# Performance work log

Hardware: AMD Instinct MI355X
Metric: run time of the kernel (lower is better)

Reference implementation:

```python
import jax, jax.numpy as jnp
import numpy as np

D = 1024
H = 16
HD = D // H
DS = 64
B, L = 2, 2048


def setup_inputs() -> dict:
    key = jax.random.key(0)
    ks = jax.random.split(key, 12)
    s = 0.02
    return {
        "x": jax.random.normal(ks[0], (B, L, D), jnp.float32),
        "subject_embed": jax.random.normal(ks[1], (B, DS), jnp.float32),
        "key_padding_mask": jnp.zeros((B, L), jnp.bool_),
        "Wq": jax.random.normal(ks[2], (D, D), jnp.float32) * s,
        "Wk": jax.random.normal(ks[3], (D, D), jnp.float32) * s,
        "Wv": jax.random.normal(ks[4], (D, D), jnp.float32) * s,
        "Wo": jax.random.normal(ks[5], (D, D), jnp.float32) * s,
        "bo": jnp.zeros((D,), jnp.float32),
        "Wsq": jax.random.normal(ks[6], (DS, D), jnp.float32) * s,
        "bsq": jnp.zeros((D,), jnp.float32),
        "Wsk": jax.random.normal(ks[7], (DS, D), jnp.float32) * s,
        "bsk": jnp.zeros((D,), jnp.float32),
    }


def reference(x, subject_embed, key_padding_mask, Wq, Wk, Wv, Wo, bo, Wsq, bsq, Wsk, bsk):
    scale = 1.0 / jnp.sqrt(jnp.asarray(HD, x.dtype))
    q = x @ Wq + (subject_embed @ Wsq + bsq)[:, None, :]   # [B,L,D]
    k = x @ Wk + (subject_embed @ Wsk + bsk)[:, None, :]
    v = x @ Wv
    # split heads: [B,H,L,hd]
    q = q.reshape(B, L, H, HD).transpose(0, 2, 1, 3)
    k = k.reshape(B, L, H, HD).transpose(0, 2, 1, 3)
    v = v.reshape(B, L, H, HD).transpose(0, 2, 1, 3)
    attn = jnp.einsum('bhqd,bhkd->bhqk', q, k) * scale      # [B,H,L,L]
    attn = jnp.where(key_padding_mask[:, None, None, :], -jnp.inf, attn)
    attn = jax.nn.softmax(attn, axis=-1)
    out = jnp.einsum('bhqk,bhkd->bhqd', attn, v)
    out = out.transpose(0, 2, 1, 3).reshape(B, L, D)
    return out @ Wo + bo
```

## Files before the change

kernel.cpp:

```cpp
#include <hip/hip_runtime.h>
#include <hip/hip_bf16.h>
#include <math.h>

#define DEV __device__ __forceinline__

typedef short bf16x8 __attribute__((ext_vector_type(8)));
typedef short bf16x4 __attribute__((ext_vector_type(4)));
typedef float f32x4 __attribute__((ext_vector_type(4)));

static constexpr int D  = 1024;
static constexpr int H  = 16;
static constexpr int HD = 64;
static constexpr int DS = 64;
static constexpr int B  = 2;
static constexpr int L  = 2048;
static constexpr int M  = B * L;

static constexpr float QSCALE = 0.18033688011112042f;

DEV unsigned short f2bf(float f) {
  union { float f; unsigned u; } x; x.f = f;
  unsigned r = (x.u + 0x7FFFu + ((x.u >> 16) & 1u)) >> 16;
  return (unsigned short)r;
}

DEV unsigned pack2bf(float a, float b) {
  return (unsigned)f2bf(a) | ((unsigned)f2bf(b) << 16);
}

DEV unsigned pack2bf_trunc(float a, float b) {
  union { float f; unsigned u; } ua{a}, ub{b};
  return __builtin_amdgcn_perm(ub.u, ua.u, 0x07060302u);
}

DEV void gload_lds16(const void* g, void* l) {
  __builtin_amdgcn_global_load_lds(
      (const __attribute__((address_space(1))) unsigned int*)g,
      (__attribute__((address_space(3))) unsigned int*)l, 16, 0, 0);
}

__global__ __launch_bounds__(256) void prep_kernel(
    const float* __restrict__ Wq, const float* __restrict__ Wk,
    const float* __restrict__ Wv, const float* __restrict__ Wo,
    const float* __restrict__ x, const float* __restrict__ subj,
    const float* __restrict__ Wsq, const float* __restrict__ bsq,
    const float* __restrict__ Wsk, const float* __restrict__ bsk,
    unsigned short* __restrict__ WT4, unsigned short* __restrict__ xb,
    float* __restrict__ sq, float* __restrict__ sk) {
  __shared__ float tile[64][65];
  const int blk = blockIdx.x, t = threadIdx.x;
  if (blk < 1024) {
    const int z = blk >> 8, idx = blk & 255;
    const float* W = z == 0 ? Wq : z == 1 ? Wk : z == 2 ? Wv : Wo;
    unsigned short* dst = WT4 + (size_t)z * D * D;
    const int n0 = (idx & 15) * 64, k0 = (idx >> 4) * 64;
    const int c = t & 63, r4 = t >> 6;
#pragma unroll
    for (int rr = 0; rr < 16; ++rr) {
      int row = r4 + rr * 4;
      tile[row][c] = W[(size_t)(k0 + row) * D + n0 + c];
    }
    __syncthreads();
#pragma unroll
    for (int rr = 0; rr < 16; ++rr) {
      int nrow = r4 + rr * 4;
      dst[(size_t)(n0 + nrow) * D + k0 + c] = f2bf(tile[c][nrow]);
    }
  } else if (blk < 3072) {
    size_t g = (size_t)(blk - 1024) * 256 + t;
    const float4* xf = (const float4*)x;
    float4 a = xf[2 * g], b = xf[2 * g + 1];
    union { unsigned short s[8]; uint4 v; } o;
    o.s[0] = f2bf(a.x); o.s[1] = f2bf(a.y); o.s[2] = f2bf(a.z); o.s[3] = f2bf(a.w);
    o.s[4] = f2bf(b.x); o.s[5] = f2bf(b.y); o.s[6] = f2bf(b.z); o.s[7] = f2bf(b.w);
    ((uint4*)xb)[g] = o.v;
  } else {
    int g = (blk - 3072) * 256 + t;
    int ty = g >> 11, b = (g >> 10) & 1, n = g & 1023;
    const float* W = ty ? Wsk : Wsq;
    const float* bias = ty ? bsk : bsq;
    float s = bias[n];
#pragma unroll 8
    for (int d = 0; d < DS; ++d) s += subj[b * DS + d] * W[d * D + n];
    (ty ? sk : sq)[b * D + n] = s;
  }
}

__global__ __launch_bounds__(256) void proj_kernel(
    const unsigned short* __restrict__ xb, const unsigned short* __restrict__ WT3,
    const float* __restrict__ sq, const float* __restrict__ sk,
    unsigned short* __restrict__ qk, unsigned short* __restrict__ vT) {
  __shared__ __align__(16) unsigned short smem[32768];
  const int lin = blockIdx.x + 8 * (blockIdx.y + 32 * blockIdx.z);
  const int nlin = (lin & 7) * 96 + (lin >> 3);
  const int z = nlin >> 8;
  const int rem = nlin & 255;
  const unsigned short* Wt = WT3 + (size_t)z * D * D;
  const int m0 = (rem >> 3) * 128, n0 = (rem & 7) * 128;
  const int t = threadIdx.x, l = t & 63, w = t >> 6;
  const int wm = w >> 1, wn = w & 1;
  const int lm = l & 15, lq = l >> 4;
  const int srow8 = t >> 3;
  const int fsw = ((t & 7) ^ ((t >> 3) & 7)) * 8;
  const int swm = lm & 7;

  auto stage = [&](int kt, int bsel) {
    const int kb = kt * 64;
    unsigned short* As = smem + bsel * 16384;
    unsigned short* Bs = As + 8192;
#pragma unroll
    for (int c = 0; c < 4; ++c) {
      int row = 32 * c + srow8;
      gload_lds16(&xb[(size_t)(m0 + row) * D + kb + fsw], &As[(32 * c + 8 * w) * 64]);
      gload_lds16(&Wt[(size_t)(n0 + row) * D + kb + fsw], &Bs[(32 * c + 8 * w) * 64]);
    }
  };

  f32x4 acc[4][4] = {};
  stage(0, 0);
  __syncthreads();
  for (int kt = 0; kt < D / 64; ++kt) {
    const int cur = kt & 1;
    if (kt + 1 < D / 64) stage(kt + 1, cur ^ 1);
    const unsigned short* As = smem + cur * 16384;
    const unsigned short* Bs = As + 8192;
#pragma unroll
    for (int kk = 0; kk < 2; ++kk) {
      bf16x8 af[4], bf[4];
#pragma unroll
      for (int i = 0; i < 4; ++i)
        af[i] = *(const bf16x8*)&As[(64 * wm + 16 * i + lm) * 64 + ((kk * 4 + lq) ^ swm) * 8];
#pragma unroll
      for (int j = 0; j < 4; ++j)
        bf[j] = *(const bf16x8*)&Bs[(64 * wn + 16 * j + lm) * 64 + ((kk * 4 + lq) ^ swm) * 8];
#pragma unroll
      for (int i = 0; i < 4; ++i)
#pragma unroll
        for (int j = 0; j < 4; ++j)
          acc[i][j] = __builtin_amdgcn_mfma_f32_16x16x32_bf16(af[i], bf[j], acc[i][j], 0, 0, 0);
    }
    __syncthreads();
  }
  if (z == 2) {
#pragma unroll
    for (int i = 0; i < 4; ++i)
#pragma unroll
      for (int j = 0; j < 4; ++j) {
        int cr = 64 * wn + 16 * j + lm;
        int rr = 64 * wm + 16 * i + 4 * lq;
        uint2 u;
        u.x = pack2bf(acc[i][j][0], acc[i][j][1]);
        u.y = pack2bf(acc[i][j][2], acc[i][j][3]);
        *(uint2*)&smem[cr * 136 + rr] = u;
      }
    __syncthreads();
    const int cr = t >> 1, half = t & 1;
    const int bb = m0 >> 11, l0 = m0 & (L - 1);
    const int gcol = n0 + cr, h = gcol >> 6, hd = gcol & 63;
    size_t dbase = ((size_t)(bb * H + h) * HD + hd) * L + l0 + half * 64;
#pragma unroll
    for (int c = 0; c < 8; ++c) {
      uint4 u = *(const uint4*)&smem[cr * 136 + half * 64 + c * 8];
      *(uint4*)&vT[dbase + c * 8] = u;
    }
  } else {
    unsigned short* dst = qk + (size_t)z * M * D;
    const float* bias = z == 0 ? sq : sk;
    const float post = z == 0 ? QSCALE : 1.0f;
#pragma unroll
    for (int i = 0; i < 4; ++i)
#pragma unroll
      for (int j = 0; j < 4; ++j)
#pragma unroll
        for (int r = 0; r < 4; ++r) {
          int rr = 64 * wm + 16 * i + 4 * lq + r;
          int cc = 64 * wn + 16 * j + lm;
          float v = (acc[i][j][r] + bias[((m0 + rr) >> 11) * D + n0 + cc]) * post;
          smem[rr * 136 + cc] = f2bf(v);
        }
    __syncthreads();
    const int row = t >> 1, half = t & 1;
    const int bb = m0 >> 11, ll = (m0 & (L - 1)) + row;
    const int h0 = (n0 >> 6) + half;
    size_t dbase = ((size_t)(bb * H + h0) * L + ll) * HD;
#pragma unroll
    for (int c = 0; c < 8; ++c) {
      uint4 u = *(const uint4*)&smem[row * 136 + half * 64 + c * 8];
      *(uint4*)&dst[dbase + c * 8] = u;
    }
  }
}

__global__ __launch_bounds__(512, 4) void attn_kernel(
    const unsigned short* __restrict__ q_hm, const unsigned short* __restrict__ k_hm,
    const unsigned short* __restrict__ vT, const unsigned char* __restrict__ mask,
    unsigned short* __restrict__ ctx) {
  __shared__ __align__(16) unsigned short smem[40960];
  unsigned short* Qs  = smem;
  unsigned short* Ksb = smem + 8192;
  unsigned short* Vtb = smem + 24576;
  const int bx = blockIdx.x;
  const int rest = bx >> 3;
  const int bhid = (bx & 7) + 8 * (rest >> 4);
  const int q0 = (rest & 15) * 128;
  const int h = bhid & 15, b = bhid >> 4;
  const size_t bh = (size_t)(b * H + h);
  const unsigned short* qp = q_hm + bh * L * HD;
  const unsigned short* kp = k_hm + bh * L * HD;
  const unsigned short* vp = vT + bh * HD * L;
  const int t = threadIdx.x, l = t & 63, w = t >> 6;
  const int wq = w & 3, wj = w >> 2;
  const int lm = l & 15, lq = l >> 4;
  const int fsw = ((t & 7) ^ ((t >> 3) & 7)) * 8;
  const int swm = lm & 7;
  const int srow = t >> 3;
  const int vs = t & 15, vr = t >> 4;
  const int vcsrc = ((vs & 8) | ((vs & 7) ^ (vr & 7))) * 8;
  const int krow0 = 8 * (lm >> 2) + 4 * ((lm >> 2) & 1) + (lm & 3);
  const int ks0 = krow0 & 7;
  const int krow1 = krow0 ^ 4;
  const int ks1 = ks0 ^ 4;
  const bf16x8 vones = {(short)0x3F80, (short)0x3F80, (short)0x3F80, (short)0x3F80,
                        (short)0x3F80, (short)0x3F80, (short)0x3F80, (short)0x3F80};

#pragma unroll
  for (int c = 0; c < 2; ++c) {
    gload_lds16(&qp[(size_t)(q0 + 64 * c + srow) * HD + fsw], &Qs[(64 * c + 8 * w) * 64]);
    gload_lds16(&kp[(size_t)(64 * c + srow) * HD + fsw], &Ksb[(64 * c + 8 * w) * 64]);
    gload_lds16(&vp[(size_t)(32 * c + vr) * L + vcsrc], &Vtb[(32 * c + 4 * w) * 128]);
  }
  __syncthreads();
  bf16x8 qf[2][2];
#pragma unroll
  for (int i = 0; i < 2; ++i)
#pragma unroll
    for (int kk = 0; kk < 2; ++kk)
      qf[i][kk] = *(const bf16x8*)&Qs[(wq * 32 + 16 * i + lm) * 64 + ((kk * 4 + lq) ^ swm) * 8];

  f32x4 ot[2][4] = {};
  f32x4 ot1[2] = {};

  for (int kt = 0; kt < L / 128; ++kt) {
    const int cur = kt & 1;
    const unsigned short* Kc = Ksb + cur * 8192;
    const unsigned short* Vc = Vtb + cur * 8192;
    unsigned char mby = mask[b * L + kt * 128 + 64 * wj + l];
    if (kt + 1 < L / 128) {
      const int nk0 = (kt + 1) * 128;
      unsigned short* Kd = Ksb + (cur ^ 1) * 8192;
      unsigned short* Vd = Vtb + (cur ^ 1) * 8192;
#pragma unroll
      for (int c = 0; c < 2; ++c) {
        gload_lds16(&kp[(size_t)(nk0 + 64 * c + srow) * HD + fsw], &Kd[(64 * c + 8 * w) * 64]);
        gload_lds16(&vp[(size_t)(32 * c + vr) * L + nk0 + vcsrc], &Vd[(32 * c + 4 * w) * 128]);
      }
    }
    unsigned long long mb = __ballot(mby != 0);

#pragma unroll
    for (int g = 0; g < 2; ++g) {
      const int gg = 2 * wj + g;
      const unsigned short* Kg = Kc + 32 * gg * 64;
      bf16x8 ka0 = *(const bf16x8*)&Kg[krow0 * 64 + ((0 + lq) ^ ks0) * 8];
      bf16x8 ka1 = *(const bf16x8*)&Kg[krow0 * 64 + ((4 + lq) ^ ks0) * 8];
      bf16x8 kb0 = *(const bf16x8*)&Kg[krow1 * 64 + ((0 + lq) ^ ks1) * 8];
      bf16x8 kb1 = *(const bf16x8*)&Kg[krow1 * 64 + ((4 + lq) ^ ks1) * 8];
      f32x4 stA[2], stB[2];
      __builtin_amdgcn_s_setprio(1);
#pragma unroll
      for (int i = 0; i < 2; ++i) {
        f32x4 a = {};
        a = __builtin_amdgcn_mfma_f32_16x16x32_bf16(ka0, qf[i][0], a, 0, 0, 0);
        a = __builtin_amdgcn_mfma_f32_16x16x32_bf16(ka1, qf[i][1], a, 0, 0, 0);
        stA[i] = a;
        f32x4 bq = {};
        bq = __builtin_amdgcn_mfma_f32_16x16x32_bf16(kb0, qf[i][0], bq, 0, 0, 0);
        bq = __builtin_amdgcn_mfma_f32_16x16x32_bf16(kb1, qf[i][1], bq, 0, 0, 0);
        stB[i] = bq;
      }
      __builtin_amdgcn_s_setprio(0);
      if (mb) {
        const int shA = 32 * g + 8 * lq + 4 * (lq & 1);
        unsigned bitsA = (unsigned)(mb >> shA);
        unsigned bitsB = (unsigned)(mb >> (shA ^ 4));
#pragma unroll
        for (int i = 0; i < 2; ++i)
#pragma unroll
          for (int r = 0; r < 4; ++r) {
            if ((bitsA >> r) & 1u) stA[i][r] = -1e30f;
            if ((bitsB >> r) & 1u) stB[i][r] = -1e30f;
          }
      }
      union { uint4 q; bf16x8 v; } pa[2];
      const bool sw = (lq & 1) != 0;
#pragma unroll
      for (int i = 0; i < 2; ++i) {
        float eA[4], eB[4];
#pragma unroll
        for (int r = 0; r < 4; ++r) {
          eA[r] = __builtin_amdgcn_exp2f(stA[i][r]);
          eB[r] = __builtin_amdgcn_exp2f(stB[i][r]);
        }
        unsigned a01 = pack2bf_trunc(eA[0], eA[1]);
        unsigned a23 = pack2bf_trunc(eA[2], eA[3]);
        unsigned b01 = pack2bf_trunc(eB[0], eB[1]);
        unsigned b23 = pack2bf_trunc(eB[2], eB[3]);
        pa[i].q.x = sw ? b01 : a01;
        pa[i].q.y = sw ? b23 : a23;
        pa[i].q.z = sw ? a01 : b01;
        pa[i].q.w = sw ? a23 : b23;
      }
      const int kc = 4 * gg + lq;
      const int slot = (kc & 8) | ((kc & 7) ^ swm);
      __builtin_amdgcn_s_setprio(1);
#pragma unroll
      for (int jf = 0; jf < 4; ++jf) {
        bf16x8 vb = *(const bf16x8*)&Vc[(16 * jf + lm) * 128 + slot * 8];
#pragma unroll
        for (int i = 0; i < 2; ++i)
          ot[i][jf] = __builtin_amdgcn_mfma_f32_16x16x32_bf16(pa[i].v, vb, ot[i][jf], 0, 0, 0);
      }
#pragma unroll
      for (int i = 0; i < 2; ++i)
        ot1[i] = __builtin_amdgcn_mfma_f32_16x16x32_bf16(pa[i].v, vones, ot1[i], 0, 0, 0);
      __builtin_amdgcn_s_setprio(0);
    }
    __syncthreads();
  }

  float* Obuf = (float*)smem;
  unsigned short* Es = smem + 20480;
  float* Sred = (float*)(smem + 35840);

  if (lm == 0) {
#pragma unroll
    for (int i = 0; i < 2; ++i)
#pragma unroll
      for (int r = 0; r < 4; ++r)
        Sred[w * 32 + 16 * i + 4 * lq + r] = ot1[i][r];
  }
  if (wj) {
#pragma unroll
    for (int i = 0; i < 2; ++i)
#pragma unroll
      for (int jf = 0; jf < 4; ++jf)
        *(f32x4*)&Obuf[(16 * jf + lm) * 132 + wq * 32 + 16 * i + 4 * lq] = ot[i][jf];
  }
  __syncthreads();
  if (!wj) {
    float rlq[2][4];
#pragma unroll
    for (int i = 0; i < 2; ++i)
#pragma unroll
      for (int r = 0; r < 4; ++r)
        rlq[i][r] = 1.0f / (ot1[i][r] + Sred[(w + 4) * 32 + 16 * i + 4 * lq + r]);
#pragma unroll
    for (int i = 0; i < 2; ++i)
#pragma unroll
      for (int jf = 0; jf < 4; ++jf) {
        f32x4 po = *(const f32x4*)&Obuf[(16 * jf + lm) * 132 + wq * 32 + 16 * i + 4 * lq];
        ot[i][jf] += po;
      }
#pragma unroll
    for (int i = 0; i < 2; ++i)
#pragma unroll
      for (int jf = 0; jf < 4; ++jf)
#pragma unroll
        for (int r = 0; r < 4; ++r)
          Es[(wq * 32 + 16 * i + 4 * lq + r) * 72 + 16 * jf + lm] =
              f2bf(ot[i][jf][r] * rlq[i][r]);
    int row = l >> 1, half = l & 1;
    size_t obase = ((size_t)(b * L + q0 + wq * 32 + row)) * D + h * HD + half * 32;
#pragma unroll
    for (int c = 0; c < 4; ++c) {
      uint4 u = *(const uint4*)&Es[(wq * 32 + row) * 72 + half * 32 + c * 8];
      *(uint4*)&ctx[obase + c * 8] = u;
    }
  }
}

__global__ __launch_bounds__(256) void outgemm_kernel(
    const unsigned short* __restrict__ ctx, const unsigned short* __restrict__ WoT,
    const float* __restrict__ bo, float* __restrict__ out) {
  __shared__ __align__(16) unsigned short smem[24576];
  const int lin = blockIdx.x + 8 * blockIdx.y;
  const int nlin = (lin & 7) * 64 + (lin >> 3);
  const int m0 = (nlin >> 3) * 64, n0 = (nlin & 7) * 128;
  const int t = threadIdx.x, l = t & 63, w = t >> 6;
  const int wm = w >> 1, wn = w & 1;
  const int lm = l & 15, lq = l >> 4;
  const int srow8 = t >> 3;
  const int fsw = ((t & 7) ^ ((t >> 3) & 7)) * 8;
  const int swm = lm & 7;

  auto stage = [&](int kt, int bsel) {
    const int kb = kt * 64;
    unsigned short* As = smem + bsel * 12288;
    unsigned short* Bs = As + 4096;
#pragma unroll
    for (int c = 0; c < 2; ++c)
      gload_lds16(&ctx[(size_t)(m0 + 32 * c + srow8) * D + kb + fsw],
                  &As[(32 * c + 8 * w) * 64]);
#pragma unroll
    for (int c = 0; c < 4; ++c)
      gload_lds16(&WoT[(size_t)(n0 + 32 * c + srow8) * D + kb + fsw],
                  &Bs[(32 * c + 8 * w) * 64]);
  };

  f32x4 acc[2][4] = {};
  stage(0, 0);
  __syncthreads();
  for (int kt = 0; kt < D / 64; ++kt) {
    const int cur = kt & 1;
    if (kt + 1 < D / 64) stage(kt + 1, cur ^ 1);
    const unsigned short* As = smem + cur * 12288;
    const unsigned short* Bs = As + 4096;
#pragma unroll
    for (int kk = 0; kk < 2; ++kk) {
      bf16x8 af[2], bf[4];
#pragma unroll
      for (int i = 0; i < 2; ++i)
        af[i] = *(const bf16x8*)&As[(32 * wm + 16 * i + lm) * 64 + ((kk * 4 + lq) ^ swm) * 8];
#pragma unroll
      for (int j = 0; j < 4; ++j)
        bf[j] = *(const bf16x8*)&Bs[(64 * wn + 16 * j + lm) * 64 + ((kk * 4 + lq) ^ swm) * 8];
#pragma unroll
      for (int i = 0; i < 2; ++i)
#pragma unroll
        for (int j = 0; j < 4; ++j)
          acc[i][j] = __builtin_amdgcn_mfma_f32_16x16x32_bf16(af[i], bf[j], acc[i][j], 0, 0, 0);
    }
    __syncthreads();
  }
#pragma unroll
  for (int i = 0; i < 2; ++i)
#pragma unroll
    for (int j = 0; j < 4; ++j)
#pragma unroll
      for (int r = 0; r < 4; ++r) {
        int grow = m0 + 32 * wm + 16 * i + lq * 4 + r;
        int gcol = n0 + 64 * wn + 16 * j + lm;
        out[(size_t)grow * D + gcol] = acc[i][j][r] + bo[gcol];
      }
}

extern "C" void kernel_launch(void* const* d_in, const int* in_sizes, int n_in,
                              void* d_out, int out_size, void* d_ws, size_t ws_size,
                              hipStream_t stream) {
  const float* x    = (const float*)d_in[0];
  const float* subj = (const float*)d_in[1];
  const unsigned char* mask = (const unsigned char*)d_in[2];
  const float* Wq = (const float*)d_in[3];
  const float* Wk = (const float*)d_in[4];
  const float* Wv = (const float*)d_in[5];
  const float* Wo = (const float*)d_in[6];
  const float* bo = (const float*)d_in[7];
  const float* Wsq = (const float*)d_in[8];
  const float* bsq = (const float*)d_in[9];
  const float* Wsk = (const float*)d_in[10];
  const float* bsk = (const float*)d_in[11];
  float* out = (float*)d_out;
  char* ws = (char*)d_ws;

  unsigned short* xb  = (unsigned short*)(ws);
  unsigned short* WT4 = (unsigned short*)(ws + (8ull  << 20));
  unsigned short* qk  = (unsigned short*)(ws + (16ull << 20));
  unsigned short* ctx = (unsigned short*)(ws + (32ull << 20));
  unsigned short* vT  = (unsigned short*)(ws + (40ull << 20));
  float* sq = (float*)(ws + (48ull << 20));
  float* sk = sq + B * D;

  hipLaunchKernelGGL(prep_kernel, dim3(3088), dim3(256), 0, stream,
                     Wq, Wk, Wv, Wo, x, subj, Wsq, bsq, Wsk, bsk, WT4, xb, sq, sk);
  hipLaunchKernelGGL(proj_kernel, dim3(8, 32, 3), dim3(256), 0, stream,
                     xb, WT4, sq, sk, qk, vT);
  hipLaunchKernelGGL(attn_kernel, dim3(512), dim3(512), 0, stream,
                     qk, qk + (size_t)M * D, vT, mask, ctx);
  hipLaunchKernelGGL(outgemm_kernel, dim3(8, 64, 1), dim3(256), 0, stream, ctx,
                     WT4 + 3ull * D * D, bo, out);
}
```

Measured before the change: 189.6 us.

## Replace double-buffered direct-to-LDS loads with register-staged single-buffer pipeline in projection

The projection GEMM stops using double-buffered global-to-LDS direct loads. It now prefetches the next K tile into registers while computing on a single LDS buffer, then writes the registers to LDS after a barrier. This cuts LDS use per block, which may raise occupancy, but it adds a second barrier per iteration and costs extra registers for staging.

```diff
diff --git a/kernel.cpp b/kernel.cpp
--- a/kernel.cpp
+++ b/kernel.cpp
@@ -90,7 +90,9 @@
     const unsigned short* __restrict__ xb, const unsigned short* __restrict__ WT3,
     const float* __restrict__ sq, const float* __restrict__ sk,
     unsigned short* __restrict__ qk, unsigned short* __restrict__ vT) {
-  __shared__ __align__(16) unsigned short smem[32768];
+  __shared__ __align__(16) unsigned short smem[128 * 136];
+  unsigned short* As = smem;
+  unsigned short* Bs = smem + 128 * 64;
   const int lin = blockIdx.x + 8 * (blockIdx.y + 32 * blockIdx.z);
   const int nlin = (lin & 7) * 96 + (lin >> 3);
   const int z = nlin >> 8;
@@ -104,26 +106,29 @@
   const int fsw = ((t & 7) ^ ((t >> 3) & 7)) * 8;
   const int swm = lm & 7;
 
-  auto stage = [&](int kt, int bsel) {
+  uint4 ra[4], rb[4];
+  auto issue = [&](int kt) {
     const int kb = kt * 64;
-    unsigned short* As = smem + bsel * 16384;
-    unsigned short* Bs = As + 8192;
 #pragma unroll
     for (int c = 0; c < 4; ++c) {
-      int row = 32 * c + srow8;
-      gload_lds16(&xb[(size_t)(m0 + row) * D + kb + fsw], &As[(32 * c + 8 * w) * 64]);
-      gload_lds16(&Wt[(size_t)(n0 + row) * D + kb + fsw], &Bs[(32 * c + 8 * w) * 64]);
+      ra[c] = *(const uint4*)&xb[(size_t)(m0 + 32 * c + srow8) * D + kb + fsw];
+      rb[c] = *(const uint4*)&Wt[(size_t)(n0 + 32 * c + srow8) * D + kb + fsw];
     }
   };
+  auto commit = [&]() {
+#pragma unroll
+    for (int c = 0; c < 4; ++c) {
+      *(uint4*)&As[(32 * c + 8 * w) * 64 + l * 8] = ra[c];
+      *(uint4*)&Bs[(32 * c + 8 * w) * 64 + l * 8] = rb[c];
+    }
+  };
 
   f32x4 acc[4][4] = {};
-  stage(0, 0);
+  issue(0);
+  commit();
   __syncthreads();
   for (int kt = 0; kt < D / 64; ++kt) {
-    const int cur = kt & 1;
-    if (kt + 1 < D / 64) stage(kt + 1, cur ^ 1);
-    const unsigned short* As = smem + cur * 16384;
-    const unsigned short* Bs = As + 8192;
+    if (kt + 1 < D / 64) issue(kt + 1);
 #pragma unroll
     for (int kk = 0; kk < 2; ++kk) {
       bf16x8 af[4], bf[4];
@@ -140,6 +145,10 @@
           acc[i][j] = __builtin_amdgcn_mfma_f32_16x16x32_bf16(af[i], bf[j], acc[i][j], 0, 0, 0);
     }
     __syncthreads();
+    if (kt + 1 < D / 64) {
+      commit();
+      __syncthreads();
+    }
   }
   if (z == 2) {
 #pragma unroll
```

Measured after the change: 270.7 us. +42.8%, slower.
